# Performance work log

Measured on AMD Instinct MI355X. Metric: run time of the kernel, lower is better.

Reference implementation:

```python
import jax, jax.numpy as jnp
import numpy as np

WS = 32          # window_size
STRIDE = 16
OUTPUT = 224
GRADE_N = 6

def _dct_mat(size):
    i = np.arange(size)[:, None]
    j = np.arange(size)[None, :]
    scale = np.where(i == 0, np.sqrt(1.0 / size), np.sqrt(2.0 / size))
    return (scale * np.cos((j + 0.5) * np.pi * i / size)).astype(np.float32)

def _gen_filter(start, end, size):
    i = np.arange(size)[:, None]
    j = np.arange(size)[None, :]
    s = i + j
    return np.where((s > end) | (s < start), 0.0, 1.0).astype(np.float32)

# constant (non-learnable) buffers, derived from init hyperparams
_D = jnp.asarray(_dct_mat(WS))                       # [32,32]
_LEVEL_FILT = jnp.asarray(_gen_filter(0, WS * 2, WS))  # level_fliter=[0] -> band (0, 64)
_grade_filts = np.stack([_gen_filter(WS * 2.0 / GRADE_N * i, WS * 2.0 / GRADE_N * (i + 1), WS)
                         for i in range(GRADE_N)])    # [G,32,32]
_ft_num = _grade_filts.sum(axis=(1, 2))               # per-filter normalizer
_weights = (2.0 ** np.arange(GRADE_N)).astype(np.float32)  # w=1, *=2 each pass
_GRADE_FILT_SCALED = jnp.asarray(_grade_filts * (_weights / _ft_num)[:, None, None])  # [G,32,32]

def _unfold(x):
    # x: [B,C,H,W] -> patches [B,L,C,ws,ws], L row-major over (oh, ow), matching torch Unfold
    B, C, H, W = x.shape
    nH = (H - WS) // STRIDE + 1
    nW = (W - WS) // STRIDE + 1
    r = jnp.arange(nH) * STRIDE
    c = jnp.arange(nW) * STRIDE
    rows = r[:, None, None, None] + jnp.arange(WS)[None, None, :, None]  # [nH,1,ws,1]
    cols = c[None, :, None, None] + jnp.arange(WS)[None, None, None, :]  # [1,nW,1,ws]
    p = x[:, :, rows, cols]                       # [B,C,nH,nW,ws,ws]
    p = jnp.transpose(p, (0, 2, 3, 1, 4, 5))      # [B,nH,nW,C,ws,ws]
    return p.reshape(B, nH * nW, C, WS, WS)

def setup_inputs() -> dict:
    key = jax.random.key(0)
    x = jax.random.normal(key, (16, 3, 512, 512), dtype=jnp.float32)
    return {"x": x}

def reference(x):
    B, C, H, W = x.shape
    patches = _unfold(x)                          # [B,L,C,32,32]
    x_dct = _D @ patches @ _D.T                   # batched 32x32 DCT

    # level branch (level_N=1): filter is all-pass band (0,64) but applied faithfully
    level_y = _D.T @ (x_dct * _LEVEL_FILT) @ _D   # [B,L,C,32,32]

    # grading: sum_g w_g/ft_g * sum_{c,i,j} filt_g * log(|dct|+1)
    lx = jnp.log(jnp.abs(x_dct) + 1.0)
    grade = jnp.einsum('blcij,gij->bl', lx, _GRADE_FILT_SCALED)  # [B,L]

    idx = jnp.argsort(grade, axis=-1)             # ascending
    b = jnp.arange(B)
    minmin_i  = idx[:, 0]
    minmin_i1 = idx[:, 1]    # B > 1 branch
    maxmax_i  = idx[:, -1]
    maxmax_i1 = idx[:, -2]   # B > 1 branch

    # gather single patch per image; fold0 with one block == reshape to [B,C,32,32]
    x_minmin  = level_y[b, minmin_i]
    x_maxmax  = level_y[b, maxmax_i]
    x_minmin1 = level_y[b, minmin_i1]
    x_maxmax1 = level_y[b, maxmax_i1]
    return (x_minmin, x_maxmax, x_minmin1, x_maxmax1)
```

## Files before the change

### kernel.cpp

```cpp
#include <hip/hip_runtime.h>
#include <cstdint>

typedef _Float16 f16x8 __attribute__((ext_vector_type(8)));
typedef float    f32x4 __attribute__((ext_vector_type(4)));

constexpr double kPI  = 3.14159265358979323846264338327950288;
constexpr double kLN2 = 0.69314718055994530941723212145818;
constexpr double cos_poly(double x) {
    double x2 = x * x, term = 1.0, sum = 1.0;
    for (int n = 1; n <= 13; ++n) { term *= -x2 / double((2 * n - 1) * (2 * n)); sum += term; }
    return sum;
}
constexpr double cos_idx(int a) {
    a &= 127;
    if (a <= 32)  return  cos_poly(a * kPI / 64.0);
    if (a <= 64)  return -cos_poly((64 - a) * kPI / 64.0);
    if (a <= 96)  return -cos_poly((a - 64) * kPI / 64.0);
    return cos_poly((128 - a) * kPI / 64.0);
}
constexpr double csqrt(double v) {
    double x = 1.0;
    for (int i = 0; i < 60; ++i) x = 0.5 * (x + v / x);
    return x;
}
struct DTab { float d[1024]; };
constexpr DTab make_D() {
    DTab t{};
    const double s0 = csqrt(1.0 / 32.0);
    for (int i = 0; i < 32; ++i) {
        double sc = (i == 0) ? s0 : 0.25;
        for (int j = 0; j < 32; ++j)
            t.d[i * 32 + j] = (float)(sc * cos_idx(((2 * j + 1) * i) & 127));
    }
    return t;
}
struct FTab { float f[64]; };
constexpr FTab make_F() {
    FTab t{};
    const int lo[6] = {0, 11, 22, 32, 43, 54};
    const int hi[6] = {10, 21, 32, 42, 53, 62};
    const int n [6] = {66, 187, 306, 286, 165, 45};
    for (int s = 0; s < 64; ++s) {
        double acc = 0.0, w = 1.0;
        for (int g = 0; g < 6; ++g) { if (s >= lo[g] && s <= hi[g]) acc += w / double(n[g]); w *= 2.0; }
        t.f[s] = (float)(acc * kLN2);
    }
    return t;
}
__device__ constexpr DTab cD = make_D();
__device__ constexpr FTab cF = make_F();

#define NP  15376
#define NPC 46128
#define LPB 961
#define TP  36

__global__ __launch_bounds__(128) void k_init(_Float16* __restrict__ dfrag) {
    const int t = threadIdx.x;
    const int tile = t >> 6, lane = t & 63;
    const int m  = 16 * tile + (lane & 15);
    const int k0 = ((lane >> 4) & 3) * 8;
    #pragma unroll
    for (int j = 0; j < 8; ++j)
        dfrag[t * 8 + j] = (_Float16)cD.d[m * 32 + k0 + j];
}

__global__ __launch_bounds__(128, 4) void k_grade(const float* __restrict__ x,
                                                  const _Float16* __restrict__ dfrag,
                                                  float* __restrict__ partial) {
    __shared__ __align__(16) float sT[2][32 * TP];
    __shared__ float sF[64];
    const int tid  = threadIdx.x;
    const int wv   = tid >> 6, lane = tid & 63;
    const int quad = lane >> 4, n = lane & 15;
    if (tid < 64) sF[tid] = cF.f[tid];

    const int tc   = blockIdx.x * 2 + wv;
    const int task = tc / 3, c = tc - task * 3;
    const int b  = task / LPB, l = task - b * LPB;
    const int ph = l / 31, pw = l - ph * 31;

    const f16x8* DF = (const f16x8*)dfrag;
    const f16x8 d0 = DF[lane], d1 = DF[64 + lane];

    const float* pp = x + (size_t)(b * 3 + c) * 262144
                        + (size_t)(ph * 16 + quad * 8) * 512 + pw * 16 + n;
    f16x8 p0, p1;
    #pragma unroll
    for (int j = 0; j < 8; ++j) {
        p0[j] = (_Float16)pp[j * 512];
        p1[j] = (_Float16)pp[j * 512 + 16];
    }

    const f32x4 z4 = {0.f, 0.f, 0.f, 0.f};
    f32x4 t00 = __builtin_amdgcn_mfma_f32_16x16x32_f16(d0, p0, z4, 0, 0, 0);
    f32x4 t01 = __builtin_amdgcn_mfma_f32_16x16x32_f16(d0, p1, z4, 0, 0, 0);
    f32x4 t10 = __builtin_amdgcn_mfma_f32_16x16x32_f16(d1, p0, z4, 0, 0, 0);
    f32x4 t11 = __builtin_amdgcn_mfma_f32_16x16x32_f16(d1, p1, z4, 0, 0, 0);

    float* S = sT[wv];
    #pragma unroll
    for (int r = 0; r < 4; ++r) {
        S[(quad * 4 + r) * TP + n]           = t00[r];
        S[(quad * 4 + r) * TP + 16 + n]      = t01[r];
        S[(16 + quad * 4 + r) * TP + n]      = t10[r];
        S[(16 + quad * 4 + r) * TP + 16 + n] = t11[r];
    }
    __syncthreads();

    f16x8 a0, a1;
    {
        const float* rp = &S[n * TP + quad * 8];
        const float4 x0 = *(const float4*)(rp);
        const float4 x1 = *(const float4*)(rp + 4);
        const float4 x2 = *(const float4*)(rp + 16 * TP);
        const float4 x3 = *(const float4*)(rp + 16 * TP + 4);
        a0[0]=(_Float16)x0.x; a0[1]=(_Float16)x0.y; a0[2]=(_Float16)x0.z; a0[3]=(_Float16)x0.w;
        a0[4]=(_Float16)x1.x; a0[5]=(_Float16)x1.y; a0[6]=(_Float16)x1.z; a0[7]=(_Float16)x1.w;
        a1[0]=(_Float16)x2.x; a1[1]=(_Float16)x2.y; a1[2]=(_Float16)x2.z; a1[3]=(_Float16)x2.w;
        a1[4]=(_Float16)x3.x; a1[5]=(_Float16)x3.y; a1[6]=(_Float16)x3.z; a1[7]=(_Float16)x3.w;
    }

    f32x4 q00 = __builtin_amdgcn_mfma_f32_16x16x32_f16(a0, d0, z4, 0, 0, 0);
    f32x4 q01 = __builtin_amdgcn_mfma_f32_16x16x32_f16(a0, d1, z4, 0, 0, 0);
    f32x4 q10 = __builtin_amdgcn_mfma_f32_16x16x32_f16(a1, d0, z4, 0, 0, 0);
    f32x4 q11 = __builtin_amdgcn_mfma_f32_16x16x32_f16(a1, d1, z4, 0, 0, 0);

    const int sb = quad * 4 + n;
    float W[12];
    #pragma unroll
    for (int t2 = 0; t2 < 3; ++t2)
        #pragma unroll
        for (int r = 0; r < 4; ++r) W[t2 * 4 + r] = sF[sb + 16 * t2 + r];

    float gsum = 0.f;
    #pragma unroll
    for (int r = 0; r < 4; ++r) {
        gsum = fmaf(__log2f(fabsf(q00[r]) + 1.f), W[r],     gsum);
        gsum = fmaf(__log2f(fabsf(q01[r]) + 1.f), W[4 + r], gsum);
        gsum = fmaf(__log2f(fabsf(q10[r]) + 1.f), W[4 + r], gsum);
        gsum = fmaf(__log2f(fabsf(q11[r]) + 1.f), W[8 + r], gsum);
    }
    #pragma unroll
    for (int off = 32; off > 0; off >>= 1) gsum += __shfl_down(gsum, off, 64);
    if (lane == 0) partial[tc] = gsum;
}

__global__ __launch_bounds__(256) void k_selgather(const float* __restrict__ partial,
                                                   const float* __restrict__ x,
                                                   float* __restrict__ out) {
    __shared__ unsigned long long smx1[256], smx2[256], smn1[256], smn2[256];
    __shared__ int ssel[4];
    const int b = blockIdx.x, tid = threadIdx.x;
    unsigned long long mx1 = 0, mx2 = 0, mn1 = ~0ULL, mn2 = ~0ULL;
    for (int l = tid; l < LPB; l += 256) {
        const float* pp = partial + (size_t)(b * LPB + l) * 3;
        float gr = pp[0] + pp[1] + pp[2];
        unsigned int bits = __float_as_uint(gr);
        unsigned long long k = ((unsigned long long)bits << 32) | (unsigned int)l;
        if (k > mx1) { mx2 = mx1; mx1 = k; } else if (k > mx2) { mx2 = k; }
        if (k < mn1) { mn2 = mn1; mn1 = k; } else if (k < mn2) { mn2 = k; }
    }
    smx1[tid] = mx1; smx2[tid] = mx2; smn1[tid] = mn1; smn2[tid] = mn2;
    for (int off = 128; off > 0; off >>= 1) {
        __syncthreads();
        if (tid < off) {
            unsigned long long a1 = smx1[tid], a2 = smx2[tid], b1 = smx1[tid + off], b2 = smx2[tid + off];
            unsigned long long lo = a1 < b1 ? a1 : b1, hi = a1 < b1 ? b1 : a1;
            unsigned long long c2 = a2 > b2 ? a2 : b2;
            smx1[tid] = hi; smx2[tid] = lo > c2 ? lo : c2;
            a1 = smn1[tid]; a2 = smn2[tid]; b1 = smn1[tid + off]; b2 = smn2[tid + off];
            lo = a1 < b1 ? a1 : b1; hi = a1 < b1 ? b1 : a1;
            c2 = a2 < b2 ? a2 : b2;
            smn1[tid] = lo; smn2[tid] = hi < c2 ? hi : c2;
        }
    }
    __syncthreads();
    if (tid == 0) {
        ssel[0] = (int)(smn1[0] & 0xffffffffu);
        ssel[1] = (int)(smx1[0] & 0xffffffffu);
        ssel[2] = (int)(smn2[0] & 0xffffffffu);
        ssel[3] = (int)(smx2[0] & 0xffffffffu);
    }
    __syncthreads();

    #pragma unroll
    for (int it = 0; it < 12; ++it) {
        const int q  = it * 256 + tid;
        const int o  = q / 768;
        const int r2 = q - o * 768;
        const int c  = r2 >> 8;
        const int p  = r2 & 255;
        const int i  = p >> 3, j4 = p & 7;
        const int l  = ssel[o];
        const int r0 = (l / 31) * 16, c0 = (l - (l / 31) * 31) * 16;
        const float4 v = *(const float4*)(x + ((size_t)(b * 3 + c) * 512 + r0 + i) * 512 + c0 + 4 * j4);
        *(float4*)(out + (size_t)o * 49152 + b * 3072 + c * 1024 + i * 32 + 4 * j4) = v;
    }
}

extern "C" void kernel_launch(void* const* d_in, const int* in_sizes, int n_in,
                              void* d_out, int out_size, void* d_ws, size_t ws_size,
                              hipStream_t stream) {
    const float* x = (const float*)d_in[0];
    float* out     = (float*)d_out;
    float* partial = (float*)d_ws;
    _Float16* dfrag = (_Float16*)((char*)d_ws + 47104 * 4);
    k_init     <<<1,       128, 0, stream>>>(dfrag);
    k_grade    <<<NPC / 2, 128, 0, stream>>>(x, dfrag, partial);
    k_selgather<<<16,      256, 0, stream>>>(partial, x, out);
}
```

Baseline: 106.2 us.

## Process all three channels per wave with prefetch of next channel loads

The grading kernel now assigns one patch to a single 64-thread block and loops over the three channels. It prefetches the next channel's pixels into registers while the current channel's DCT runs. This also lets the sum over channels happen in-kernel, so the select kernel reads one value per patch instead of three. In exchange, the block count triples down to one per patch, each block runs longer, and an extra barrier is added per channel iteration.

```diff
diff --git a/kernel.cpp b/kernel.cpp
--- a/kernel.cpp
+++ b/kernel.cpp
@@ -1,8 +1,8 @@
 #include <hip/hip_runtime.h>
 #include <cstdint>
 
-typedef _Float16 f16x8 __attribute__((ext_vector_type(8)));
-typedef float    f32x4 __attribute__((ext_vector_type(4)));
+typedef _Float16 f16x8  __attribute__((ext_vector_type(8)));
+typedef float    f32x4  __attribute__((ext_vector_type(4)));
 
 constexpr double kPI  = 3.14159265358979323846264338327950288;
 constexpr double kLN2 = 0.69314718055994530941723212145818;
@@ -51,7 +51,6 @@
 __device__ constexpr FTab cF = make_F();
 
 #define NP  15376
-#define NPC 46128
 #define LPB 961
 #define TP  36
 
@@ -65,67 +64,23 @@
         dfrag[t * 8 + j] = (_Float16)cD.d[m * 32 + k0 + j];
 }
 
-__global__ __launch_bounds__(128, 4) void k_grade(const float* __restrict__ x,
-                                                  const _Float16* __restrict__ dfrag,
-                                                  float* __restrict__ partial) {
-    __shared__ __align__(16) float sT[2][32 * TP];
+__global__ __launch_bounds__(64, 4) void k_grade(const float* __restrict__ x,
+                                                 const _Float16* __restrict__ dfrag,
+                                                 float* __restrict__ partial) {
+    __shared__ __align__(16) float sT[32 * TP];
     __shared__ float sF[64];
-    const int tid  = threadIdx.x;
-    const int wv   = tid >> 6, lane = tid & 63;
+    const int lane = threadIdx.x & 63;
     const int quad = lane >> 4, n = lane & 15;
-    if (tid < 64) sF[tid] = cF.f[tid];
-
-    const int tc   = blockIdx.x * 2 + wv;
-    const int task = tc / 3, c = tc - task * 3;
+    sF[lane] = cF.f[lane];
+
+    const int task = blockIdx.x;
     const int b  = task / LPB, l = task - b * LPB;
-    const int ph = l / 31, pw = l - ph * 31;
+    const int ph = l / 31,     pw = l - ph * 31;
 
     const f16x8* DF = (const f16x8*)dfrag;
     const f16x8 d0 = DF[lane], d1 = DF[64 + lane];
 
-    const float* pp = x + (size_t)(b * 3 + c) * 262144
-                        + (size_t)(ph * 16 + quad * 8) * 512 + pw * 16 + n;
-    f16x8 p0, p1;
-    #pragma unroll
-    for (int j = 0; j < 8; ++j) {
-        p0[j] = (_Float16)pp[j * 512];
-        p1[j] = (_Float16)pp[j * 512 + 16];
-    }
-
-    const f32x4 z4 = {0.f, 0.f, 0.f, 0.f};
-    f32x4 t00 = __builtin_amdgcn_mfma_f32_16x16x32_f16(d0, p0, z4, 0, 0, 0);
-    f32x4 t01 = __builtin_amdgcn_mfma_f32_16x16x32_f16(d0, p1, z4, 0, 0, 0);
-    f32x4 t10 = __builtin_amdgcn_mfma_f32_16x16x32_f16(d1, p0, z4, 0, 0, 0);
-    f32x4 t11 = __builtin_amdgcn_mfma_f32_16x16x32_f16(d1, p1, z4, 0, 0, 0);
-
-    float* S = sT[wv];
-    #pragma unroll
-    for (int r = 0; r < 4; ++r) {
-        S[(quad * 4 + r) * TP + n]           = t00[r];
-        S[(quad * 4 + r) * TP + 16 + n]      = t01[r];
-        S[(16 + quad * 4 + r) * TP + n]      = t10[r];
-        S[(16 + quad * 4 + r) * TP + 16 + n] = t11[r];
-    }
     __syncthreads();
-
-    f16x8 a0, a1;
-    {
-        const float* rp = &S[n * TP + quad * 8];
-        const float4 x0 = *(const float4*)(rp);
-        const float4 x1 = *(const float4*)(rp + 4);
-        const float4 x2 = *(const float4*)(rp + 16 * TP);
-        const float4 x3 = *(const float4*)(rp + 16 * TP + 4);
-        a0[0]=(_Float16)x0.x; a0[1]=(_Float16)x0.y; a0[2]=(_Float16)x0.z; a0[3]=(_Float16)x0.w;
-        a0[4]=(_Float16)x1.x; a0[5]=(_Float16)x1.y; a0[6]=(_Float16)x1.z; a0[7]=(_Float16)x1.w;
-        a1[0]=(_Float16)x2.x; a1[1]=(_Float16)x2.y; a1[2]=(_Float16)x2.z; a1[3]=(_Float16)x2.w;
-        a1[4]=(_Float16)x3.x; a1[5]=(_Float16)x3.y; a1[6]=(_Float16)x3.z; a1[7]=(_Float16)x3.w;
-    }
-
-    f32x4 q00 = __builtin_amdgcn_mfma_f32_16x16x32_f16(a0, d0, z4, 0, 0, 0);
-    f32x4 q01 = __builtin_amdgcn_mfma_f32_16x16x32_f16(a0, d1, z4, 0, 0, 0);
-    f32x4 q10 = __builtin_amdgcn_mfma_f32_16x16x32_f16(a1, d0, z4, 0, 0, 0);
-    f32x4 q11 = __builtin_amdgcn_mfma_f32_16x16x32_f16(a1, d1, z4, 0, 0, 0);
-
     const int sb = quad * 4 + n;
     float W[12];
     #pragma unroll
@@ -133,17 +88,70 @@
         #pragma unroll
         for (int r = 0; r < 4; ++r) W[t2 * 4 + r] = sF[sb + 16 * t2 + r];
 
+    const float* pbase = x + (size_t)(b * 3) * 262144
+                           + (size_t)(ph * 16 + quad * 8) * 512 + pw * 16 + n;
+    float pv[16];
+    #pragma unroll
+    for (int j = 0; j < 8; ++j) { pv[j] = pbase[j * 512]; pv[8 + j] = pbase[j * 512 + 16]; }
+
+    const f32x4 z4 = {0.f, 0.f, 0.f, 0.f};
     float gsum = 0.f;
-    #pragma unroll
-    for (int r = 0; r < 4; ++r) {
-        gsum = fmaf(__log2f(fabsf(q00[r]) + 1.f), W[r],     gsum);
-        gsum = fmaf(__log2f(fabsf(q01[r]) + 1.f), W[4 + r], gsum);
-        gsum = fmaf(__log2f(fabsf(q10[r]) + 1.f), W[4 + r], gsum);
-        gsum = fmaf(__log2f(fabsf(q11[r]) + 1.f), W[8 + r], gsum);
+
+    #pragma unroll
+    for (int c = 0; c < 3; ++c) {
+        f16x8 p0, p1;
+        #pragma unroll
+        for (int j = 0; j < 8; ++j) { p0[j] = (_Float16)pv[j]; p1[j] = (_Float16)pv[8 + j]; }
+        if (c < 2) {
+            const float* nb = pbase + (size_t)(c + 1) * 262144;
+            #pragma unroll
+            for (int j = 0; j < 8; ++j) { pv[j] = nb[j * 512]; pv[8 + j] = nb[j * 512 + 16]; }
+        }
+
+        f32x4 t00 = __builtin_amdgcn_mfma_f32_16x16x32_f16(d0, p0, z4, 0, 0, 0);
+        f32x4 t01 = __builtin_amdgcn_mfma_f32_16x16x32_f16(d0, p1, z4, 0, 0, 0);
+        f32x4 t10 = __builtin_amdgcn_mfma_f32_16x16x32_f16(d1, p0, z4, 0, 0, 0);
+        f32x4 t11 = __builtin_amdgcn_mfma_f32_16x16x32_f16(d1, p1, z4, 0, 0, 0);
+
+        #pragma unroll
+        for (int r = 0; r < 4; ++r) {
+            sT[(quad * 4 + r) * TP + n]           = t00[r];
+            sT[(quad * 4 + r) * TP + 16 + n]      = t01[r];
+            sT[(16 + quad * 4 + r) * TP + n]      = t10[r];
+            sT[(16 + quad * 4 + r) * TP + 16 + n] = t11[r];
+        }
+        __syncthreads();
+
+        f16x8 a0, a1;
+        {
+            const float* rp = &sT[n * TP + quad * 8];
+            const float4 x0 = *(const float4*)(rp);
+            const float4 x1 = *(const float4*)(rp + 4);
+            const float4 x2 = *(const float4*)(rp + 16 * TP);
+            const float4 x3 = *(const float4*)(rp + 16 * TP + 4);
+            a0[0]=(_Float16)x0.x; a0[1]=(_Float16)x0.y; a0[2]=(_Float16)x0.z; a0[3]=(_Float16)x0.w;
+            a0[4]=(_Float16)x1.x; a0[5]=(_Float16)x1.y; a0[6]=(_Float16)x1.z; a0[7]=(_Float16)x1.w;
+            a1[0]=(_Float16)x2.x; a1[1]=(_Float16)x2.y; a1[2]=(_Float16)x2.z; a1[3]=(_Float16)x2.w;
+            a1[4]=(_Float16)x3.x; a1[5]=(_Float16)x3.y; a1[6]=(_Float16)x3.z; a1[7]=(_Float16)x3.w;
+        }
+        __syncthreads();
+
+        f32x4 q00 = __builtin_amdgcn_mfma_f32_16x16x32_f16(a0, d0, z4, 0, 0, 0);
+        f32x4 q01 = __builtin_amdgcn_mfma_f32_16x16x32_f16(a0, d1, z4, 0, 0, 0);
+        f32x4 q10 = __builtin_amdgcn_mfma_f32_16x16x32_f16(a1, d0, z4, 0, 0, 0);
+        f32x4 q11 = __builtin_amdgcn_mfma_f32_16x16x32_f16(a1, d1, z4, 0, 0, 0);
+
+        #pragma unroll
+        for (int r = 0; r < 4; ++r) {
+            gsum = fmaf(__log2f(fabsf(q00[r]) + 1.f), W[r],     gsum);
+            gsum = fmaf(__log2f(fabsf(q01[r]) + 1.f), W[4 + r], gsum);
+            gsum = fmaf(__log2f(fabsf(q10[r]) + 1.f), W[4 + r], gsum);
+            gsum = fmaf(__log2f(fabsf(q11[r]) + 1.f), W[8 + r], gsum);
+        }
     }
     #pragma unroll
     for (int off = 32; off > 0; off >>= 1) gsum += __shfl_down(gsum, off, 64);
-    if (lane == 0) partial[tc] = gsum;
+    if (lane == 0) partial[task] = gsum;
 }
 
 __global__ __launch_bounds__(256) void k_selgather(const float* __restrict__ partial,
@@ -154,9 +162,7 @@
     const int b = blockIdx.x, tid = threadIdx.x;
     unsigned long long mx1 = 0, mx2 = 0, mn1 = ~0ULL, mn2 = ~0ULL;
     for (int l = tid; l < LPB; l += 256) {
-        const float* pp = partial + (size_t)(b * LPB + l) * 3;
-        float gr = pp[0] + pp[1] + pp[2];
-        unsigned int bits = __float_as_uint(gr);
+        unsigned int bits = __float_as_uint(partial[b * LPB + l]);
         unsigned long long k = ((unsigned long long)bits << 32) | (unsigned int)l;
         if (k > mx1) { mx2 = mx1; mx1 = k; } else if (k > mx2) { mx2 = k; }
         if (k < mn1) { mn2 = mn1; mn1 = k; } else if (k < mn2) { mn2 = k; }
@@ -205,8 +211,8 @@
     const float* x = (const float*)d_in[0];
     float* out     = (float*)d_out;
     float* partial = (float*)d_ws;
-    _Float16* dfrag = (_Float16*)((char*)d_ws + 47104 * 4);
-    k_init     <<<1,       128, 0, stream>>>(dfrag);
-    k_grade    <<<NPC / 2, 128, 0, stream>>>(x, dfrag, partial);
-    k_selgather<<<16,      256, 0, stream>>>(partial, x, out);
-}
+    _Float16* dfrag = (_Float16*)((char*)d_ws + 61504);
+    k_init     <<<1,  128, 0, stream>>>(dfrag);
+    k_grade    <<<NP,  64, 0, stream>>>(x, dfrag, partial);
+    k_selgather<<<16, 256, 0, stream>>>(partial, x, out);
+}
```

After: 107.0 us. No clear change (+0.8%).
